# Performance work log

Measured on AMD Instinct MI355X. Metric: run time of the kernel, lower is better.

Reference implementation:

```python
import jax, jax.numpy as jnp
import numpy as np

F, HE, HD, A = 128, 512, 512, 256
B, T = 32, 512

def _uniform(key, shape, k):
    return jax.random.uniform(key, shape, jnp.float32, -k, k)

def setup_inputs() -> dict:
    key = jax.random.key(0)
    ks = jax.random.split(key, 20)
    ke = 1.0 / np.sqrt(HE)
    kd = 1.0 / np.sqrt(HD)
    ka = 1.0 / np.sqrt(A)
    kf = 1.0 / np.sqrt(F)
    return {
        "x": jax.random.normal(ks[0], (B, T, F), jnp.float32),
        # encoder LSTM (torch gate order i,f,g,o)
        "enc_Wih": _uniform(ks[1], (4 * HE, F), ke),
        "enc_Whh": _uniform(ks[2], (4 * HE, HE), ke),
        "enc_bih": _uniform(ks[3], (4 * HE,), ke),
        "enc_bhh": _uniform(ks[4], (4 * HE,), ke),
        # attention
        "Wenc_w": _uniform(ks[5], (A, HE), 1.0 / np.sqrt(HE)),
        "Wenc_b": _uniform(ks[6], (A,), 1.0 / np.sqrt(HE)),
        "Wdec_w": _uniform(ks[7], (A, HD), kd),
        "Wdec_b": _uniform(ks[8], (A,), kd),
        "V_w": _uniform(ks[9], (1, A), ka),
        "V_b": _uniform(ks[10], (1,), ka),
        "attn_bias": _uniform(ks[11], (A,), kd),
        # decoder LSTMCell: input size HD+HE
        "dec_Wih": _uniform(ks[12], (4 * HD, HD + HE), kd),
        "dec_Whh": _uniform(ks[13], (4 * HD, HD), kd),
        "dec_bih": _uniform(ks[14], (4 * HD,), kd),
        "dec_bhh": _uniform(ks[15], (4 * HD,), kd),
    }

def _lstm_step(xw, h, c, Whh, bias, H):
    # xw = x @ Wih.T precomputed; bias = bih + bhh
    z = xw + h @ Whh.T + bias
    i, f, g, o = jnp.split(z, 4, axis=-1)
    i, f, o = jax.nn.sigmoid(i), jax.nn.sigmoid(f), jax.nn.sigmoid(o)
    g = jnp.tanh(g)
    c_new = f * c + i * g
    h_new = o * jnp.tanh(c_new)
    return h_new, c_new

def reference(x, enc_Wih, enc_Whh, enc_bih, enc_bhh,
              Wenc_w, Wenc_b, Wdec_w, Wdec_b, V_w, V_b, attn_bias,
              dec_Wih, dec_Whh, dec_bih, dec_bhh):
    nb, nt, _ = x.shape
    # ---- encoder LSTM ----
    xw = jnp.einsum('btf,gf->btg', x, enc_Wih)  # [B,T,4HE]
    enc_bias = enc_bih + enc_bhh
    def enc_step(carry, xw_t):
        h, c = carry
        h, c = _lstm_step(xw_t, h, c, enc_Whh, enc_bias, HE)
        return (h, c), h
    h0 = jnp.zeros((nb, HE), x.dtype)
    c0 = jnp.zeros((nb, HE), x.dtype)
    _, enc_states = jax.lax.scan(enc_step, (h0, c0), jnp.swapaxes(xw, 0, 1))
    enc_states = jnp.swapaxes(enc_states, 0, 1)  # [B,T,HE]

    # ---- initial decoder step: zero input, zero state ----
    dec_bias = dec_bih + dec_bhh
    z0 = jnp.broadcast_to(dec_bias, (nb, 4 * HD))
    i, f, g, o = jnp.split(z0, 4, axis=-1)
    cdec = jax.nn.sigmoid(i) * jnp.tanh(g)
    hdec = jax.nn.sigmoid(o) * jnp.tanh(cdec)

    # precompute encoder projection for attention (math identical to per-step)
    enc_proj = jnp.einsum('bte,ae->bta', enc_states, Wenc_w) + Wenc_b  # [B,T,A]

    def dec_step(carry, _):
        h, c = carry
        dscore = h @ Wdec_w.T + Wdec_b  # [B,A]
        align = jnp.tanh(enc_proj + dscore[:, None, :] + attn_bias)  # [B,T,A]
        logits = jnp.einsum('bta,a->bt', align, V_w[0]) + V_b[0]
        w = jax.nn.softmax(logits, axis=-1)  # [B,T]
        ctx = jnp.einsum('bt,bte->be', w, enc_states)  # [B,HE]
        dec_in = jnp.concatenate([ctx, h], axis=-1)
        h, c = _lstm_step(dec_in @ dec_Wih.T, h, c, dec_Whh, dec_bias, HD)
        return (h, c), h
    _, outs = jax.lax.scan(dec_step, (hdec, cdec), None, length=nt)
    return jnp.swapaxes(outs, 0, 1)  # [B,T,HD]
```

## Files before the change

### kernel.cpp

```cpp
#include <hip/hip_runtime.h>
#include <stdint.h>

#define DEV __device__ __forceinline__

namespace {

constexpr int kT = 512, kB = 32, kF = 128, kHE = 512, kHD = 512, kA = 256;

typedef _Float16 f16;
typedef _Float16 h4 __attribute__((ext_vector_type(4)));
typedef unsigned long long u64;

constexpr size_t oWdecC  = 0;
constexpr size_t oWdWH   = oWdecC + 1048576;
constexpr size_t oEncSt  = oWdWH + 65536;
constexpr size_t oEncPr  = oEncSt + (size_t)kB*kT*kHE;
constexpr size_t oHdec   = oEncPr + (size_t)kB*kT*kA;
constexpr size_t oCtx    = oHdec + 3ull*kB*kHD;
constexpr size_t oDen    = oCtx + 3ull*kB*kHE;
constexpr size_t oScp    = oDen + 96;
constexpr size_t oEbias  = oScp + (size_t)kB*16*kA;
constexpr size_t oDbias  = oEbias + 2048;
constexpr size_t oAb2    = oDbias + 2048;
constexpr size_t oCtr    = oAb2 + 256;
constexpr size_t oHenc   = oCtr + 2048;
constexpr size_t oCtxP   = oEncSt;
constexpr size_t oDenP   = oEncSt + 3ull*32*16*512;

constexpr float kScale = 1.0f/64.0f;

DEV float frcp(float x){ return __builtin_amdgcn_rcpf(x); }
DEV float fsig(float x){ return frcp(1.f + __expf(-x)); }
DEV float ftanh(float x){ return 1.f - 2.f*frcp(__expf(2.f*x) + 1.f); }

DEV float ld_na(const float* p){ return __hip_atomic_load((float*)p, __ATOMIC_RELAXED, __HIP_MEMORY_SCOPE_AGENT); }
DEV void  st_na(float* p, float v){ __hip_atomic_store(p, v, __ATOMIC_RELAXED, __HIP_MEMORY_SCOPE_AGENT); }
DEV int   ld_ni(const int* p){ return __hip_atomic_load((int*)p, __ATOMIC_RELAXED, __HIP_MEMORY_SCOPE_AGENT); }
DEV void  st_ni(int* p, int v){ __hip_atomic_store(p, v, __ATOMIC_RELAXED, __HIP_MEMORY_SCOPE_AGENT); }
DEV float2 ld_na2(const float* p){
  u64 v = __hip_atomic_load((const u64*)p, __ATOMIC_RELAXED, __HIP_MEMORY_SCOPE_AGENT);
  union { u64 u; float2 f; } cv; cv.u = v; return cv.f;
}
DEV void st_na2(float* p, float2 v){
  union { float2 f; u64 u; } cv; cv.f = v;
  __hip_atomic_store((u64*)p, cv.u, __ATOMIC_RELAXED, __HIP_MEMORY_SCOPE_AGENT);
}

DEV void wait_slots(const int* base, int cnt, int tgt, int* abortf){
  if (threadIdx.x < 64){
    int lane = threadIdx.x;
    int guard = 0;
    for (;;){
      int ok = 1;
      for (int i = lane; i < cnt; i += 64) ok &= (ld_ni(base + i) >= tgt);
      if (__all(ok)) break;
      if (ld_ni(abortf) != 0) break;
      if (++guard > (1<<21)){ st_ni(abortf, 1); break; }
      __builtin_amdgcn_s_sleep(1);
    }
  }
  __syncthreads();
}
DEV void wait_count(const int* p, int tgt, int* abortf){
  if (threadIdx.x < 64){
    int guard = 0;
    for (;;){
      if (ld_ni(p) >= tgt) break;
      if (ld_ni(abortf) != 0) break;
      if (++guard > (1<<21)){ st_ni(abortf, 1); break; }
      __builtin_amdgcn_s_sleep(2);
    }
  }
  __syncthreads();
}
DEV void stamp_slot(int* slot, int v){
  __syncthreads();
  if (threadIdx.x == 0) st_ni(slot, v);
}

}

__global__ __launch_bounds__(256) void init_kernel(
    const float* __restrict__ eBih, const float* __restrict__ eBhh,
    const float* __restrict__ WdecW, const float* __restrict__ WdecB, const float* __restrict__ attnB,
    const float* __restrict__ dWih, const float* __restrict__ dWhh,
    const float* __restrict__ dBih, const float* __restrict__ dBhh,
    float* __restrict__ ws)
{
  float* whc = ws + oWdecC;
  f16* wdwh  = (f16*)(ws + oWdWH);
  float* hdec  = ws + oHdec;
  float* ebias = ws + oEbias;
  float* dbias = ws + oDbias;
  float* ab2w  = ws + oAb2;
  float* henc  = ws + oHenc;
  const int gid = blockIdx.x*256 + threadIdx.x;
  const int stride = gridDim.x*256;
  for (int i=gid; i<2048*512; i+=stride){
    int col = i>>9, k = i&511;
    whc[i] = dWih[((size_t)col<<10) + 512 + k] + dWhh[((size_t)col<<9) + k];
  }
  for (int i=gid; i<256*512; i+=stride)  wdwh[i] = (f16)WdecW[i];
  for (int i=gid; i<2048; i+=stride){ ebias[i] = eBih[i]+eBhh[i]; dbias[i] = dBih[i]+dBhh[i]; }
  for (int i=gid; i<256; i+=stride)  ab2w[i] = WdecB[i]+attnB[i];
  for (int i=gid; i<2*kB*kHE; i+=stride) henc[i] = 0.f;
  for (int i=gid; i<kB*kHD; i+=stride){
    int e = i & 511;
    float zi = dBih[e]+dBhh[e];
    float zg = dBih[1024+e]+dBhh[1024+e];
    float zo = dBih[1536+e]+dBhh[1536+e];
    float c0 = fsig(zi)*ftanh(zg);
    hdec[i] = fsig(zo)*ftanh(c0);
  }
}

__global__ __launch_bounds__(256, 1) void enc_kernel(
    const float* __restrict__ x, const float* __restrict__ eWih,
    const float* __restrict__ eWhh, float* __restrict__ ws)
{
  constexpr int WP = 644;
  constexpr int XP = 648;
  __shared__ float wsm[32*WP];
  __shared__ float xh[8*XP];
  __shared__ float zs[8][32];
  const float* ebias = ws + oEbias;
  float* encst = ws + oEncSt;
  float* henc  = ws + oHenc;
  int* ctr = (int*)(ws + oCtr);
  int* abortf = ctr;
  int* slotE = ctr + 1600;

  const int tid = threadIdx.x, bid = blockIdx.x;
  const int q = bid >> 6, j = bid & 63;
  const int b0 = q*8, e0 = j*8;

  for (int i = tid; i < 32*640; i += 256){
    int r = i / 640, k = i - r*640;
    int gate = r >> 3, el = r & 7;
    int grow = gate*kHE + e0 + el;
    float v = (k < kF) ? eWih[(size_t)grow*kF + k] : eWhh[(size_t)grow*kHE + (k - kF)];
    wsm[r*WP + k] = v;
  }
  const int b_l = tid >> 5, row = tid & 31;
  const float biasr = ebias[(row>>3)*kHE + e0 + (row&7)];
  const int b_p = tid >> 3, e_p = tid & 7;
  float creg = 0.f;
  __syncthreads();

  int p = 0;
  for (int t = 0; t < kT; ++t){
    {
      int bl2 = tid >> 5, q4 = tid & 31;
      *(float4*)(&xh[bl2*XP + 4*q4]) = ((const float4*)(x + ((size_t)(b0+bl2)*kT + t)*kF))[q4];
    }
    wait_slots(slotE + q*64, 64, t, abortf);
    #pragma unroll
    for (int i = 0; i < 4; ++i){
      int idx = tid + 256*i;
      int bl2 = idx >> 7, q4 = idx & 127;
      const float* hsrc = henc + (size_t)p*kB*kHE + (size_t)(b0+bl2)*kHE + 4*q4;
      float4 hv;
      hv.x = ld_na(hsrc); hv.y = ld_na(hsrc+1); hv.z = ld_na(hsrc+2); hv.w = ld_na(hsrc+3);
      *(float4*)(&xh[bl2*XP + kF + 4*q4]) = hv;
    }
    __syncthreads();
    {
      const float4* wr = (const float4*)(&wsm[row*WP]);
      const float4* xr = (const float4*)(&xh[b_l*XP]);
      float a0=0.f, a1=0.f, a2=0.f, a3=0.f;
      #pragma unroll 8
      for (int kq = 0; kq < 160; ++kq){
        float4 w = wr[kq], v = xr[kq];
        a0 += w.x*v.x; a1 += w.y*v.y; a2 += w.z*v.z; a3 += w.w*v.w;
      }
      zs[b_l][row] = (a0+a1)+(a2+a3) + biasr;
    }
    __syncthreads();
    if (tid < 64){
      float zi = zs[b_p][0*8 + e_p];
      float zf = zs[b_p][1*8 + e_p];
      float zg = zs[b_p][2*8 + e_p];
      float zo = zs[b_p][3*8 + e_p];
      float c2 = fsig(zf)*creg + fsig(zi)*ftanh(zg);
      creg = c2;
      float h = fsig(zo)*ftanh(c2);
      int b = b0 + b_p, e = e0 + e_p;
      st_na(&henc[(size_t)(p^1)*kB*kHE + (size_t)b*kHE + e], h);
      encst[((size_t)b*kT + t)*kHE + e] = h;
    }
    stamp_slot(&slotE[q*64 + j], t+1);
    p ^= 1;
  }
}

__global__ __launch_bounds__(256) void encproj_kernel(
    const float* __restrict__ WencW, const float* __restrict__ WencB,
    float* __restrict__ ws)
{
  const float* encst = ws + oEncSt;
  float* encpr = ws + oEncPr;
  __shared__ float4 et[32][32];
  const int tid = threadIdx.x, bid = blockIdx.x;
  const int r0 = bid*32;
  float acc[32];
  #pragma unroll
  for (int i=0;i<32;++i) acc[i]=0.f;
  for (int kt=0; kt<4; ++kt){
    #pragma unroll
    for (int i2=0;i2<4;++i2){
      int q = tid + i2*256;
      int row = q>>5, qi = q&31;
      et[row][qi] = ((const float4*)(encst + ((size_t)(r0+row))*kHE + kt*128))[qi];
    }
    __syncthreads();
    const float4* wv = (const float4*)(WencW + (size_t)tid*kHE + kt*128);
    #pragma unroll 1
    for (int q=0;q<32;++q){
      float4 w = wv[q];
      #pragma unroll
      for (int i=0;i<32;++i){
        float4 e4 = et[i][q];
        acc[i] += e4.x*w.x + e4.y*w.y + e4.z*w.z + e4.w*w.w;
      }
    }
    __syncthreads();
  }
  float bb = WencB[tid];
  #pragma unroll
  for (int i=0;i<32;++i) encpr[((size_t)(r0+i))*kA + tid] = acc[i] + bb;
}

namespace {
struct SA  { float h[32]; float sc[256]; float lw[32]; };
struct SC  { float xt[16][260]; float zb[128][2]; };
struct __align__(16) SmemDec {
  float wsl[8][1028];
  float v[256];
  SA a;
  SC c;
};
}

__global__ __launch_bounds__(256, 2) void dec_kernel(
    const float* __restrict__ Vw, const float* __restrict__ dWih,
    float* __restrict__ out, float* __restrict__ ws)
{
  __shared__ SmemDec sm;
  const int tid = threadIdx.x, bid = blockIdx.x;
  const float* whc = ws + oWdecC;
  const f16* wdwh  = (const f16*)(ws + oWdWH);
  const float* encst = ws + oEncSt;
  const float* encpr = ws + oEncPr;
  float* hdec = ws + oHdec;
  float* ctxb = ws + oCtx;
  float* den  = ws + oDen;
  float* scp  = ws + oScp;
  float* ctxp = ws + oCtxP;
  float* denp = ws + oDenP;
  const float* dbias = ws + oDbias;
  const float* ab2w  = ws + oAb2;
  int* ctr   = (int*)(ws + oCtr);
  int* abortf = ctr;
  int* startc = ctr + 16;
  int* slotC = ctr + 64;
  int* slotA = ctr + 576;
  int* slotB = ctr + 1088;
  int* slotR = ctr + 1856;

  const int bA = bid >> 4, tc = bid & 15, t0a = tc*32;
  const int half = bid >> 8, ecp = bid & 255, e0c = ecp*2;
  const bool isR = (tc == 0);
  const int col_l = tid & 127, ksC = tid >> 7;
  const int e_lC = col_l & 1, gateC = (col_l>>1)&3, b_lC = col_l>>3;
  const int wrow = gateC*2 + e_lC;

  for (int i = tid; i < 8*1024; i += 256){
    int rr = i >> 10, k = i & 1023;
    int col = (rr>>1)*kHD + e0c + (rr&1);
    float v = (k < 512) ? dWih[(size_t)col*1024 + k] : whc[(size_t)col*512 + (k-512)];
    sm.wsl[rr][k] = v;
  }
  sm.v[tid] = Vw[tid];

  h4 wA[8];
  { const h4* wv0 = (const h4*)(wdwh + (size_t)tid*kHD + t0a);
    #pragma unroll
    for (int q=0;q<8;++q) wA[q] = wv0[q]; }
  const int tl = tid>>3, as = tid&7;
  float4 eprR[8];
  { const float* eb2 = encpr + ((size_t)bA*kT + t0a + tl)*kA + as*4;
    #pragma unroll
    for (int q=0;q<8;++q) eprR[q] = *(const float4*)(eb2 + q*32); }
  float2 ev[32];
  { const float* eb = encst + ((size_t)bA*kT + t0a)*kHE + 2*tid;
    #pragma unroll
    for (int j=0;j<32;++j) ev[j] = *(const float2*)(eb + (size_t)j*kHE); }

  const float ab2r = ab2w[tid];
  float cregD=0, dbi=0, dbf=0, dbg=0, dbo=0;
  if (tid < 32){
    int e = e0c + (tid&1);
    dbi = dbias[e]; dbf = dbias[512+e]; dbg = dbias[1024+e]; dbo = dbias[1536+e];
    cregD = fsig(dbi)*ftanh(dbg);
  }
  __syncthreads();
  if (tid == 0) atomicAdd(startc, 1);
  wait_count(startc, 512, abortf);

  const int off  = (2*tid) & 255;
  const int mych = tid >> 7;

  int r = 0;
  for (int t=0; t<kT; ++t){
    const int rn = (r==2) ? 0 : r+1;
    wait_slots(slotC + (bA>>4)*256 + tc*16, 16, t, abortf);
    if (tid < 32) sm.a.h[tid] = ld_na(hdec + (size_t)r*kB*kHD + (size_t)bA*kHD + t0a + tid);
    __syncthreads();
    {
      float sp = 0.f;
      #pragma unroll
      for (int q=0;q<8;++q){
        h4 w = wA[q];
        sp += (float)w.x*sm.a.h[q*4+0] + (float)w.y*sm.a.h[q*4+1]
            + (float)w.z*sm.a.h[q*4+2] + (float)w.w*sm.a.h[q*4+3];
      }
      st_na(&scp[((size_t)bA*16 + tc)*kA + tid], sp);
    }
    stamp_slot(&slotA[bA*16 + tc], t+1);
    wait_slots(slotA + bA*16, 16, t+1, abortf);
    {
      float sc = ab2r;
      #pragma unroll
      for (int j=0;j<16;++j) sc += ld_na(&scp[((size_t)bA*16 + j)*kA + tid]);
      sm.a.sc[tid] = sc;
    }
    __syncthreads();
    {
      float acc = 0.f;
      #pragma unroll
      for (int q=0;q<8;++q){
        int a0 = q*32 + as*4;
        float4 e4 = eprR[q];
        acc += sm.v[a0+0]*ftanh(e4.x + sm.a.sc[a0+0]);
        acc += sm.v[a0+1]*ftanh(e4.y + sm.a.sc[a0+1]);
        acc += sm.v[a0+2]*ftanh(e4.z + sm.a.sc[a0+2]);
        acc += sm.v[a0+3]*ftanh(e4.w + sm.a.sc[a0+3]);
      }
      acc += __shfl_down(acc, 4, 8);
      acc += __shfl_down(acc, 2, 8);
      acc += __shfl_down(acc, 1, 8);
      if (as == 0) sm.a.lw[tl] = __expf(acc) * kScale;
    }
    __syncthreads();
    {
      float c0=0.f, c1=0.f;
      #pragma unroll
      for (int j=0;j<32;++j){
        float w = sm.a.lw[j];
        c0 += w*ev[j].x; c1 += w*ev[j].y;
      }
      st_na2(&ctxp[(((size_t)r*kB + bA)*16 + tc)*kHE + 2*tid], make_float2(c0, c1));
      if (tid == 0){
        float ds = 0.f;
        #pragma unroll
        for (int j=0;j<32;++j) ds += sm.a.lw[j];
        st_na(&denp[((size_t)r*kB + bA)*16 + tc], ds);
      }
    }
    stamp_slot(&slotB[bA*16 + tc], t+1);
    if (isR){
      wait_slots(slotB + bA*16, 16, t+1, abortf);
      {
        const float* pb = ctxp + ((size_t)r*kB + bA)*16*kHE + 2*tid;
        float s0=0.f, s1=0.f;
        #pragma unroll
        for (int j=0;j<16;++j){
          float2 p = ld_na2(pb + (size_t)j*kHE);
          s0 += p.x; s1 += p.y;
        }
        st_na2(&ctxb[((size_t)r*kB + bA)*kHE + 2*tid], make_float2(s0, s1));
        float d = (tid < 16) ? ld_na(&denp[((size_t)r*kB + bA)*16 + tid]) : 0.f;
        d += __shfl_down(d, 8, 16);
        d += __shfl_down(d, 4, 16);
        d += __shfl_down(d, 2, 16);
        d += __shfl_down(d, 1, 16);
        if (tid == 0) st_na(&den[r*kB + bA], d);
      }
      stamp_slot(&slotR[bA], t+1);
    }
    wait_slots(slotC + half*256, 256, t, abortf);
    float acch = 0.f;
    {
      const float* hbase = hdec + (size_t)r*kB*kHD + (size_t)(half*16)*kHD + 2*tid;
      float hux[16], huy[16];
      #pragma unroll
      for (int b=0;b<16;++b){
        float2 hv = ld_na2(hbase + (size_t)b*kHD);
        hux[b] = hv.x; huy[b] = hv.y;
      }
      #pragma unroll
      for (int kc=2; kc<4; ++kc){
        if ((kc & 1) == mych){
          #pragma unroll
          for (int b=0;b<16;++b){ sm.c.xt[b][off] = hux[b]; sm.c.xt[b][off+1] = huy[b]; }
        }
        __syncthreads();
        {
          const float4* wc4 = (const float4*)(&sm.wsl[wrow][kc*256 + ksC*128]);
          const float4* xv  = (const float4*)(&sm.c.xt[b_lC][ksC*128]);
          float a0=0.f, a1=0.f, a2=0.f, a3=0.f;
          #pragma unroll 8
          for (int q=0;q<32;++q){
            float4 w = wc4[q], v = xv[q];
            a0 += w.x*v.x; a1 += w.y*v.y; a2 += w.z*v.z; a3 += w.w*v.w;
          }
          acch += (a0+a1)+(a2+a3);
        }
        __syncthreads();
      }
    }
    wait_slots(slotR + half*16, 16, t+1, abortf);
    {
      const float rv = frcp(ld_na(&den[r*kB + half*16 + b_lC]));
      const float* cbase = ctxb + (size_t)r*kB*kHE + (size_t)(half*16)*kHE + 2*tid;
      float cux[16], cuy[16];
      #pragma unroll
      for (int b=0;b<16;++b){
        float2 cv = ld_na2(cbase + (size_t)b*kHE);
        cux[b] = cv.x; cuy[b] = cv.y;
      }
      float accc = 0.f;
      #pragma unroll
      for (int kc=0; kc<2; ++kc){
        if ((kc & 1) == mych){
          #pragma unroll
          for (int b=0;b<16;++b){ sm.c.xt[b][off] = cux[b]; sm.c.xt[b][off+1] = cuy[b]; }
        }
        __syncthreads();
        {
          const float4* wc4 = (const float4*)(&sm.wsl[wrow][kc*256 + ksC*128]);
          const float4* xv  = (const float4*)(&sm.c.xt[b_lC][ksC*128]);
          float a0=0.f, a1=0.f, a2=0.f, a3=0.f;
          #pragma unroll 8
          for (int q=0;q<32;++q){
            float4 w = wc4[q], v = xv[q];
            a0 += w.x*v.x; a1 += w.y*v.y; a2 += w.z*v.z; a3 += w.w*v.w;
          }
          accc += (a0+a1)+(a2+a3);
        }
        __syncthreads();
      }
      sm.c.zb[col_l][ksC] = accc*rv + acch;
      __syncthreads();
      if (tid < 32){
        int base = (tid>>1)*8 + (tid&1);
        int e = e0c + (tid&1), b2 = half*16 + (tid>>1);
        float zi = sm.c.zb[base+0][0] + sm.c.zb[base+0][1] + dbi;
        float zf = sm.c.zb[base+2][0] + sm.c.zb[base+2][1] + dbf;
        float zg = sm.c.zb[base+4][0] + sm.c.zb[base+4][1] + dbg;
        float zo = sm.c.zb[base+6][0] + sm.c.zb[base+6][1] + dbo;
        float c2 = fsig(zf)*cregD + fsig(zi)*ftanh(zg);
        cregD = c2;
        float h = fsig(zo)*ftanh(c2);
        st_na(&hdec[(size_t)rn*kB*kHD + (size_t)b2*kHD + e], h);
        out[((size_t)b2*kT + t)*kHD + e] = h;
      }
    }
    stamp_slot(&slotC[half*256 + ecp], t+1);
    r = rn;
  }
}

extern "C" void kernel_launch(void* const* d_in, const int* in_sizes, int n_in,
                              void* d_out, int out_size, void* d_ws, size_t ws_size,
                              hipStream_t stream) {
  (void)in_sizes; (void)n_in; (void)out_size; (void)ws_size;
  const float* x     = (const float*)d_in[0];
  const float* eWih  = (const float*)d_in[1];
  const float* eWhh  = (const float*)d_in[2];
  const float* eBih  = (const float*)d_in[3];
  const float* eBhh  = (const float*)d_in[4];
  const float* WencW = (const float*)d_in[5];
  const float* WencB = (const float*)d_in[6];
  const float* WdecW = (const float*)d_in[7];
  const float* WdecB = (const float*)d_in[8];
  const float* Vw    = (const float*)d_in[9];
  const float* attnB = (const float*)d_in[11];
  const float* dWih  = (const float*)d_in[12];
  const float* dWhh  = (const float*)d_in[13];
  const float* dBih  = (const float*)d_in[14];
  const float* dBhh  = (const float*)d_in[15];
  float* ws = (float*)d_ws;
  int* ctr = (int*)(ws + oCtr);
  hipMemsetAsync(ctr, 0, 8192, stream);
  hipLaunchKernelGGL(init_kernel, dim3(512), dim3(256), 0, stream,
                     eBih, eBhh, WdecW, WdecB, attnB, dWih, dWhh, dBih, dBhh, ws);
  hipLaunchKernelGGL(enc_kernel, dim3(256), dim3(256), 0, stream, x, eWih, eWhh, ws);
  hipLaunchKernelGGL(encproj_kernel, dim3(512), dim3(256), 0, stream, WencW, WencB, ws);
  hipLaunchKernelGGL(dec_kernel, dim3(512), dim3(256), 0, stream, Vw, dWih, (float*)d_out, ws);
}
```

Before: 14.98 ms.

## Overlap encoder x-part dot with wait, widen decoder staging to cut barriers

In the encoder, the input-projection part of the gate dot product (the first 128 elements, from x) is computed before waiting on the hidden-state slots, so it overlaps the cross-block spin. The hidden-state loads become float2 loads instead of four scalar loads. In the decoder, the staging buffer is doubled to 512 columns, so the whole h and ctx vectors are written once and each phase needs one barrier instead of alternating half-writes with two barriers per chunk. This raises decoder shared memory use by about 16 KB, which may affect the two-blocks-per-CU occupancy.

```diff
diff --git a/kernel.cpp b/kernel.cpp
--- a/kernel.cpp
+++ b/kernel.cpp
@@ -153,23 +153,31 @@
       int bl2 = tid >> 5, q4 = tid & 31;
       *(float4*)(&xh[bl2*XP + 4*q4]) = ((const float4*)(x + ((size_t)(b0+bl2)*kT + t)*kF))[q4];
     }
+    float a0=0.f, a1=0.f, a2=0.f, a3=0.f;
+    {
+      const float4* wr = (const float4*)(&wsm[row*WP]);
+      const float4* xr = (const float4*)(&xh[b_l*XP]);
+      #pragma unroll 8
+      for (int kq = 0; kq < 32; ++kq){
+        float4 w = wr[kq], v = xr[kq];
+        a0 += w.x*v.x; a1 += w.y*v.y; a2 += w.z*v.z; a3 += w.w*v.w;
+      }
+    }
     wait_slots(slotE + q*64, 64, t, abortf);
     #pragma unroll
     for (int i = 0; i < 4; ++i){
       int idx = tid + 256*i;
       int bl2 = idx >> 7, q4 = idx & 127;
       const float* hsrc = henc + (size_t)p*kB*kHE + (size_t)(b0+bl2)*kHE + 4*q4;
-      float4 hv;
-      hv.x = ld_na(hsrc); hv.y = ld_na(hsrc+1); hv.z = ld_na(hsrc+2); hv.w = ld_na(hsrc+3);
-      *(float4*)(&xh[bl2*XP + kF + 4*q4]) = hv;
+      float2 h01 = ld_na2(hsrc), h23 = ld_na2(hsrc + 2);
+      *(float4*)(&xh[bl2*XP + kF + 4*q4]) = make_float4(h01.x, h01.y, h23.x, h23.y);
     }
     __syncthreads();
     {
       const float4* wr = (const float4*)(&wsm[row*WP]);
       const float4* xr = (const float4*)(&xh[b_l*XP]);
-      float a0=0.f, a1=0.f, a2=0.f, a3=0.f;
       #pragma unroll 8
-      for (int kq = 0; kq < 160; ++kq){
+      for (int kq = 32; kq < 160; ++kq){
         float4 w = wr[kq], v = xr[kq];
         a0 += w.x*v.x; a1 += w.y*v.y; a2 += w.z*v.z; a3 += w.w*v.w;
       }
@@ -232,7 +240,7 @@
 
 namespace {
 struct SA  { float h[32]; float sc[256]; float lw[32]; };
-struct SC  { float xt[16][260]; float zb[128][2]; };
+struct SC  { float xt[16][520]; float zb[128][2]; };
 struct __align__(16) SmemDec {
   float wsl[8][1028];
   float v[256];
@@ -307,9 +315,6 @@
   if (tid == 0) atomicAdd(startc, 1);
   wait_count(startc, 512, abortf);
 
-  const int off  = (2*tid) & 255;
-  const int mych = tid >> 7;
-
   int r = 0;
   for (int t=0; t<kT; ++t){
     const int rn = (r==2) ? 0 : r+1;
@@ -392,63 +397,48 @@
     float acch = 0.f;
     {
       const float* hbase = hdec + (size_t)r*kB*kHD + (size_t)(half*16)*kHD + 2*tid;
-      float hux[16], huy[16];
-      #pragma unroll
-      for (int b=0;b<16;++b){
-        float2 hv = ld_na2(hbase + (size_t)b*kHD);
-        hux[b] = hv.x; huy[b] = hv.y;
-      }
+      float2 hu[16];
+      #pragma unroll
+      for (int b=0;b<16;++b) hu[b] = ld_na2(hbase + (size_t)b*kHD);
+      #pragma unroll
+      for (int b=0;b<16;++b) *(float2*)(&sm.c.xt[b][2*tid]) = hu[b];
+      __syncthreads();
       #pragma unroll
       for (int kc=2; kc<4; ++kc){
-        if ((kc & 1) == mych){
-          #pragma unroll
-          for (int b=0;b<16;++b){ sm.c.xt[b][off] = hux[b]; sm.c.xt[b][off+1] = huy[b]; }
+        const float4* wc4 = (const float4*)(&sm.wsl[wrow][kc*256 + ksC*128]);
+        const float4* xv  = (const float4*)(&sm.c.xt[b_lC][(kc-2)*256 + ksC*128]);
+        float a0=0.f, a1=0.f, a2=0.f, a3=0.f;
+        #pragma unroll 8
+        for (int q=0;q<32;++q){
+          float4 w = wc4[q], v = xv[q];
+          a0 += w.x*v.x; a1 += w.y*v.y; a2 += w.z*v.z; a3 += w.w*v.w;
         }
-        __syncthreads();
-        {
-          const float4* wc4 = (const float4*)(&sm.wsl[wrow][kc*256 + ksC*128]);
-          const float4* xv  = (const float4*)(&sm.c.xt[b_lC][ksC*128]);
-          float a0=0.f, a1=0.f, a2=0.f, a3=0.f;
-          #pragma unroll 8
-          for (int q=0;q<32;++q){
-            float4 w = wc4[q], v = xv[q];
-            a0 += w.x*v.x; a1 += w.y*v.y; a2 += w.z*v.z; a3 += w.w*v.w;
-          }
-          acch += (a0+a1)+(a2+a3);
-        }
-        __syncthreads();
-      }
+        acch += (a0+a1)+(a2+a3);
+      }
+      __syncthreads();
     }
     wait_slots(slotR + half*16, 16, t+1, abortf);
     {
       const float rv = frcp(ld_na(&den[r*kB + half*16 + b_lC]));
       const float* cbase = ctxb + (size_t)r*kB*kHE + (size_t)(half*16)*kHE + 2*tid;
-      float cux[16], cuy[16];
-      #pragma unroll
-      for (int b=0;b<16;++b){
-        float2 cv = ld_na2(cbase + (size_t)b*kHE);
-        cux[b] = cv.x; cuy[b] = cv.y;
-      }
+      float2 cu[16];
+      #pragma unroll
+      for (int b=0;b<16;++b) cu[b] = ld_na2(cbase + (size_t)b*kHE);
+      #pragma unroll
+      for (int b=0;b<16;++b) *(float2*)(&sm.c.xt[b][2*tid]) = cu[b];
+      __syncthreads();
       float accc = 0.f;
       #pragma unroll
       for (int kc=0; kc<2; ++kc){
-        if ((kc & 1) == mych){
-          #pragma unroll
-          for (int b=0;b<16;++b){ sm.c.xt[b][off] = cux[b]; sm.c.xt[b][off+1] = cuy[b]; }
+        const float4* wc4 = (const float4*)(&sm.wsl[wrow][kc*256 + ksC*128]);
+        const float4* xv  = (const float4*)(&sm.c.xt[b_lC][kc*256 + ksC*128]);
+        float a0=0.f, a1=0.f, a2=0.f, a3=0.f;
+        #pragma unroll 8
+        for (int q=0;q<32;++q){
+          float4 w = wc4[q], v = xv[q];
+          a0 += w.x*v.x; a1 += w.y*v.y; a2 += w.z*v.z; a3 += w.w*v.w;
         }
-        __syncthreads();
-        {
-          const float4* wc4 = (const float4*)(&sm.wsl[wrow][kc*256 + ksC*128]);
-          const float4* xv  = (const float4*)(&sm.c.xt[b_lC][ksC*128]);
-          float a0=0.f, a1=0.f, a2=0.f, a3=0.f;
-          #pragma unroll 8
-          for (int q=0;q<32;++q){
-            float4 w = wc4[q], v = xv[q];
-            a0 += w.x*v.x; a1 += w.y*v.y; a2 += w.z*v.z; a3 += w.w*v.w;
-          }
-          accc += (a0+a1)+(a2+a3);
-        }
-        __syncthreads();
+        accc += (a0+a1)+(a2+a3);
       }
       sm.c.zb[col_l][ksC] = accc*rv + acch;
       __syncthreads();
```

New measurement: 12.32 ms (median of 2 runs). -17.8%, faster.
